# Kernel optimization log

Measured on AMD Instinct MI355X. Metric: run time of the kernel, lower is better.

Reference implementation:

```python
import jax, jax.numpy as jnp
import numpy as np

D_DYN = 256    # dynamic_dim
D_STAT = 64    # static_dim
U_DIM = 48     # config.model.u_dim
N_OBS = 80     # num_prod*2 + num_inj = 32*2 + 16
T = 128        # rollout steps
B = 2048       # batch


def setup_inputs() -> dict:
    key = jax.random.key(0)
    k = jax.random.split(key, 8)
    z_dyn = jax.random.normal(k[0], (B, D_DYN), dtype=jnp.float32)
    z_static = jax.random.normal(k[1], (B, D_STAT), dtype=jnp.float32)
    dt = jnp.ones((1,), dtype=jnp.float32) * 0.05
    U = jax.random.normal(k[2], (T, B, U_DIM), dtype=jnp.float32)
    # learned params, initialized as in the torch module
    eig_raw = jnp.zeros((D_DYN,), dtype=jnp.float32)
    V = jnp.eye(D_DYN, dtype=jnp.float32) + jax.random.normal(k[3], (D_DYN, D_DYN), dtype=jnp.float32) * 0.01
    L = jax.random.normal(k[4], (D_DYN, U_DIM), dtype=jnp.float32) * (1.0 / np.sqrt(U_DIM))
    C = jax.random.normal(k[5], (N_OBS, D_DYN), dtype=jnp.float32) * (1.0 / np.sqrt(D_DYN))
    Dm = jax.random.normal(k[6], (N_OBS, U_DIM), dtype=jnp.float32) * (1.0 / np.sqrt(U_DIM))
    return {"z_dyn": z_dyn, "z_static": z_static, "dt": dt, "U": U,
            "eig_raw": eig_raw, "V": V, "L": L, "C": C, "Dm": Dm}


def reference(z_dyn, z_static, dt, U, eig_raw, V, L, C, Dm):
    # Stable Koopman operator: K = V diag(sigmoid(eig_raw)*0.99) V^{-1}
    eigvals = jax.nn.sigmoid(eig_raw) * 0.99
    K = (V * eigvals[None, :]) @ jnp.linalg.inv(V)  # [d, d]
    KT, LT, CT, DT = K.T, L.T, C.T, Dm.T
    dts = dt[0]

    def step(z, ut):
        ut_dt = ut * dts                 # [B, u_dim]
        z = z @ KT + ut_dt @ LT          # [B, d]
        y = z @ CT + ut_dt @ DT          # [B, n_obs]
        return z, (z, y)

    _, (Z, Y) = jax.lax.scan(step, z_dyn, U)
    return Z, Y  # [T, B, d], [T, B, n_obs]
```

## Files before the change

### kernel.cpp

```cpp
#include <hip/hip_runtime.h>

#define D_   256
#define UD_  48
#define NO_  80
#define T_   128
#define B_   2048

typedef __bf16 bf16x8 __attribute__((ext_vector_type(8)));
typedef float  f32x4  __attribute__((ext_vector_type(4)));
typedef unsigned short ushort_t;

static __device__ __forceinline__ ushort_t f2bf(float f){
  return __builtin_bit_cast(ushort_t, (__bf16)f);
}
static __device__ __forceinline__ float bf2f(ushort_t u){
  union { unsigned int i; float f; } c; c.i = ((unsigned int)u) << 16; return c.f;
}
static __device__ __forceinline__ f32x4 mfma16(bf16x8 a, bf16x8 b, f32x4 c){
  return __builtin_amdgcn_mfma_f32_16x16x32_bf16(a, b, c, 0, 0, 0);
}


__global__ void __launch_bounds__(256) k_pre(
    const float* __restrict__ V, const float* __restrict__ eig,
    const float* __restrict__ Cmat,
    float* __restrict__ W, float* __restrict__ Cw,
    float* __restrict__ lam, float* __restrict__ dVd){
  const int bid = blockIdx.x, tid = threadIdx.x;
  if (bid < 256){
    const float* Ar = V + bid*D_;
    float a0=0.f,a1=0.f,a2=0.f,a3=0.f;
    #pragma unroll 4
    for (int k = 0; k < D_; k += 4){
      a0 += Ar[k+0] * V[(k+0)*D_ + tid];
      a1 += Ar[k+1] * V[(k+1)*D_ + tid];
      a2 += Ar[k+2] * V[(k+2)*D_ + tid];
      a3 += Ar[k+3] * V[(k+3)*D_ + tid];
    }
    W[bid*D_ + tid] = (a0+a1)+(a2+a3);
  } else if (bid < 256 + NO_){
    const int n = bid - 256;
    float acc = 0.f;
    #pragma unroll 4
    for (int j = 0; j < D_; ++j) acc += Cmat[n*D_ + j] * V[j*D_ + tid];
    Cw[n*D_ + tid] = acc;
  } else {
    lam[tid] = 0.99f / (1.0f + expf(-eig[tid]));
    const float v = V[tid*D_ + tid];
    dVd[tid] = v - bf2f(f2bf(v));
  }
}

__global__ void __launch_bounds__(256) k_x1(
    const float* __restrict__ V, const float* __restrict__ W,
    float* __restrict__ X1){
  const int i = blockIdx.x, j = threadIdx.x;
  const float* Ar = V + i*D_;
  float a0=0.f,a1=0.f,a2=0.f,a3=0.f;
  #pragma unroll 4
  for (int k = 0; k < D_; k += 4){
    a0 += Ar[k+0] * W[(k+0)*D_ + j];
    a1 += Ar[k+1] * W[(k+1)*D_ + j];
    a2 += Ar[k+2] * W[(k+2)*D_ + j];
    a3 += Ar[k+3] * W[(k+3)*D_ + j];
  }
  X1[i*D_ + j] = (i == j ? 4.0f : 0.0f) - 6.0f*V[i*D_ + j] + 4.0f*W[i*D_ + j]
                 - ((a0+a1)+(a2+a3));
}

__global__ void __launch_bounds__(256) k_mm_mul(
    const float* __restrict__ A, const float* __restrict__ B,
    float* __restrict__ Cm){
  const int i = blockIdx.x, j = threadIdx.x;
  const float* Ar = A + i*D_;
  float a0=0.f,a1=0.f,a2=0.f,a3=0.f;
  #pragma unroll 4
  for (int k = 0; k < D_; k += 4){
    a0 += Ar[k+0] * B[(k+0)*D_ + j];
    a1 += Ar[k+1] * B[(k+1)*D_ + j];
    a2 += Ar[k+2] * B[(k+2)*D_ + j];
    a3 += Ar[k+3] * B[(k+3)*D_ + j];
  }
  Cm[i*D_ + j] = (a0+a1)+(a2+a3);
}

__global__ void __launch_bounds__(256) k_x2(
    const float* __restrict__ X1, const float* __restrict__ Tm,
    const float* __restrict__ Lmat, const float* __restrict__ dt,
    float* __restrict__ VinvT, float* __restrict__ Lw){
  __shared__ float row[256];
  const int i = blockIdx.x, j = threadIdx.x;
  const float* Xr = X1 + i*D_;
  float a0=0.f,a1=0.f,a2=0.f,a3=0.f;
  #pragma unroll 4
  for (int k = 0; k < D_; k += 4){
    a0 += Xr[k+0] * Tm[(k+0)*D_ + j];
    a1 += Xr[k+1] * Tm[(k+1)*D_ + j];
    a2 += Xr[k+2] * Tm[(k+2)*D_ + j];
    a3 += Xr[k+3] * Tm[(k+3)*D_ + j];
  }
  const float out = 2.0f*Xr[j] - ((a0+a1)+(a2+a3));
  VinvT[j*D_ + i] = out;
  row[j] = out;
  __syncthreads();
  if (j < UD_){
    float acc = 0.f;
    #pragma unroll 4
    for (int k = 0; k < D_; ++k) acc += row[k] * Lmat[k*UD_ + j];
    Lw[i*UD_ + j] = acc * dt[0];
  }
}

__global__ void __launch_bounds__(256) k_prep2(
    const float* __restrict__ z0, const float* __restrict__ VinvT,
    const float* __restrict__ Lw, const float* __restrict__ V,
    const float* __restrict__ Cw, const float* __restrict__ Dmat,
    const float* __restrict__ dt,
    ushort_t* __restrict__ Wchk, ushort_t* __restrict__ Lws,
    ushort_t* __restrict__ Af){
  __shared__ float zr[8][256];
  const int bid = blockIdx.x, tid = threadIdx.x;
  if (bid < 256){
    const int b0 = bid * 8;
    #pragma unroll
    for (int r = 0; r < 8; ++r) zr[r][tid] = z0[(size_t)(b0+r)*D_ + tid];
    __syncthreads();
    float acc[8] = {0.f,0.f,0.f,0.f,0.f,0.f,0.f,0.f};
    #pragma unroll 4
    for (int j = 0; j < D_; ++j){
      const float vj = VinvT[j*D_ + tid];
      #pragma unroll
      for (int r = 0; r < 8; ++r) acc[r] += zr[r][j] * vj;
    }
    #pragma unroll
    for (int r = 0; r < 8; ++r)
      Wchk[(size_t)(b0+r)*D_ + tid] = f2bf(acc[r]);
  } else if (bid < 288){
    const int f = bid - 256;
    if (tid < 64){
      const int l = tid, lm = l & 15, lh = l >> 4;
      const int it = f >> 1, kc2 = f & 1;
      const int ig = it*16 + lm;
      #pragma unroll
      for (int j = 0; j < 8; ++j){
        const int k = 32*kc2 + 4*lh + (j & 3) + 16*(j >> 2);
        Lws[(f*64 + l)*8 + j] = f2bf(k < UD_ ? Lw[ig*UD_ + k] : 0.f);
      }
    }
  } else {
    const int v = (bid - 288)*4 + (tid >> 6);
    if (v < 210){
      const int mt = v / 10, kc = v % 10;
      const int l = tid & 63, lm = l & 15, lh = l >> 4;
      const float dts = dt[0];
      #pragma unroll
      for (int j = 0; j < 8; ++j){
        const int k = 32*kc + 4*lh + (j & 3) + 16*(j >> 2);
        float val = 0.f;
        if (mt < 16){
          if (kc < 8) val = V[(mt*16 + lm)*D_ + k];
        } else {
          const int n = (mt - 16)*16 + lm;
          if (kc < 8) val = Cw[n*D_ + k];
          else { const int ku = k - 256; if (ku < UD_) val = dts * Dmat[n*UD_ + ku]; }
        }
        Af[((size_t)(mt*10 + kc)*64 + l)*8 + j] = f2bf(val);
      }
    }
  }
}

#define SCAN_STEP4(UA, UB, UC, TT) do {                                         \
  union { ushort_t us[8]; bf16x8 v; } c0, c1;                                   \
  c0.us[0]=f2bf((UA).x); c0.us[1]=f2bf((UA).y); c0.us[2]=f2bf((UA).z); c0.us[3]=f2bf((UA).w); \
  c0.us[4]=f2bf((UB).x); c0.us[5]=f2bf((UB).y); c0.us[6]=f2bf((UB).z); c0.us[7]=f2bf((UB).w); \
  c1.us[0]=f2bf((UC).x); c1.us[1]=f2bf((UC).y); c1.us[2]=f2bf((UC).z); c1.us[3]=f2bf((UC).w); \
  c1.us[4]=0; c1.us[5]=0; c1.us[6]=0; c1.us[7]=0;                               \
  _Pragma("unroll")                                                             \
  for (int q = 0; q < 4; ++q){                                                  \
    f32x4 acc = {0.f,0.f,0.f,0.f};                                              \
    acc = mfma16(lwf[q*2+0], c0.v, acc);                                        \
    acc = mfma16(lwf[q*2+1], c1.v, acc);                                        \
    _Pragma("unroll")                                                           \
    for (int r = 0; r < 4; ++r) w[q*4+r] = lamr[q*4+r]*w[q*4+r] + acc[r];       \
  }                                                                             \
  if ((((TT) & 7) == 7) && ((TT) < T_-1)){                                      \
    const int c2 = ((TT)+1) >> 3;                                               \
    _Pragma("unroll")                                                           \
    for (int q = 0; q < 4; ++q){                                                \
      const int i = (itb+q)*16 + 4*lh;                                          \
      ushort4 o; o.x=f2bf(w[q*4+0]); o.y=f2bf(w[q*4+1]); o.z=f2bf(w[q*4+2]); o.w=f2bf(w[q*4+3]); \
      *(ushort4*)(Wchk + ((size_t)c2*B_ + row)*D_ + i) = o;                     \
    }                                                                           \
  }                                                                             \
} while(0)

__global__ void __launch_bounds__(256) k_scan(const float* __restrict__ U,
    const ushort_t* __restrict__ Lws, const float* __restrict__ lam,
    ushort_t* __restrict__ Wchk){
  const int tid = threadIdx.x;
  const int wid = tid >> 6, l = tid & 63;
  const int lm = l & 15, lh = l >> 4;
  const int b0 = blockIdx.x * 16;
  const int row = b0 + lm;
  const int itb = wid*4;

  bf16x8 lwf[8];
  #pragma unroll
  for (int q = 0; q < 4; ++q)
    #pragma unroll
    for (int c = 0; c < 2; ++c)
      lwf[q*2 + c] = *(const bf16x8*)(Lws + ((size_t)(((itb+q)*2 + c)*64 + l))*8);

  float lamr[16], w[16];
  #pragma unroll
  for (int q = 0; q < 4; ++q){
    const int i = (itb+q)*16 + 4*lh;
    const float4 lv = *(const float4*)&lam[i];
    const ushort4 wu = *(const ushort4*)(Wchk + (size_t)row*D_ + i);
    lamr[q*4+0]=lv.x; lamr[q*4+1]=lv.y; lamr[q*4+2]=lv.z; lamr[q*4+3]=lv.w;
    w[q*4+0]=bf2f(wu.x); w[q*4+1]=bf2f(wu.y); w[q*4+2]=bf2f(wu.z); w[q*4+3]=bf2f(wu.w);
  }

  const size_t TS = (size_t)B_ * UD_;
  const float* Urow = U + (size_t)row * UD_;
  float4 Aa, Ab, Ac, Ba, Bb, Bc;
  Aa = *(const float4*)&Urow[4*lh]; Ab = *(const float4*)&Urow[16+4*lh]; Ac = *(const float4*)&Urow[32+4*lh];
  { const float* Up = Urow + TS;
    Ba = *(const float4*)&Up[4*lh]; Bb = *(const float4*)&Up[16+4*lh]; Bc = *(const float4*)&Up[32+4*lh]; }

  #pragma unroll 1
  for (int tt = 0; tt < 64; ++tt){
    const int t0 = 2*tt;
    SCAN_STEP4(Aa, Ab, Ac, t0);
    if (t0 + 2 < T_){
      const float* Up = Urow + (size_t)(t0+2)*TS;
      Aa = *(const float4*)&Up[4*lh]; Ab = *(const float4*)&Up[16+4*lh]; Ac = *(const float4*)&Up[32+4*lh];
    }
    SCAN_STEP4(Ba, Bb, Bc, t0+1);
    if (t0 + 3 < T_){
      const float* Up = Urow + (size_t)(t0+3)*TS;
      Ba = *(const float4*)&Up[4*lh]; Bb = *(const float4*)&Up[16+4*lh]; Bc = *(const float4*)&Up[32+4*lh];
    }
  }
}

__global__ void __launch_bounds__(256) k_fused(
    const float* __restrict__ U, const ushort_t* __restrict__ Af,
    const ushort_t* __restrict__ Lws, const float* __restrict__ lam,
    const float* __restrict__ dVd, const ushort_t* __restrict__ Wchk,
    float* __restrict__ outZ, float* __restrict__ outY){
  __shared__ __align__(16) ushort_t AfZhL[8*8*512];
  __shared__ __align__(16) ushort_t LwsL[32*512];
  __shared__ __align__(16) ushort_t AfYhL[40*512];
  __shared__ __align__(16) float    trbZ[4][16][68];
  __shared__ __align__(16) float    dVdL[128];
  __shared__ __align__(16) float    lamL[256];

  const int tid = threadIdx.x;
  const int bid = blockIdx.x;
  const int h  = bid & 1;
  const int ch = (bid >> 1) & 15;
  const int bq = bid >> 5;
  const int wid = tid >> 6, l = tid & 63;
  const int lm = l & 15, lh = l >> 4;
  const int col0 = bq*64 + wid*16;
  const int col = col0 + lm;

  {
    const uint4* gsrc = (const uint4*)Af;
    uint4* dz = (uint4*)AfZhL;
    #pragma unroll
    for (int r = 0; r < 16; ++r){
      const int i = r*256 + tid;
      const int f = i >> 6, l4 = i & 63;
      const int mi8 = f >> 3, kc = f & 7;
      dz[i] = gsrc[(size_t)((h*8 + mi8)*10 + kc)*64 + l4];
    }
    uint4* dy = (uint4*)AfYhL;
    const int nY = h ? 640 : 2560;
    const int sb = 16 + (h ? 4 : 0);
    #pragma unroll
    for (int r = 0; r < 10; ++r){
      const int i = r*256 + tid;
      if (i < nY){
        const int f = i >> 6, l4 = i & 63;
        const int myl = f / 10, j = f % 10;
        dy[i] = gsrc[(size_t)((sb + myl)*10 + j)*64 + l4];
      }
    }
    const uint4* ls = (const uint4*)Lws;
    uint4* ld = (uint4*)LwsL;
    #pragma unroll
    for (int r = 0; r < 8; ++r) ld[r*256 + tid] = ls[r*256 + tid];
    if (tid < 32) ((float4*)dVdL)[tid] = ((const float4*)(dVd + h*128))[tid];
    else if (tid < 96) ((float4*)lamL)[tid-32] = ((const float4*)lam)[tid-32];
  }

  float w[64];
  #pragma unroll
  for (int kc = 0; kc < 8; ++kc)
    #pragma unroll
    for (int hh = 0; hh < 2; ++hh){
      const int i = 32*kc + 16*hh + 4*lh;
      const ushort4 wu = *(const ushort4*)(Wchk + ((size_t)ch*B_ + col)*D_ + i);
      const int e = 8*kc + 4*hh;
      w[e+0]=bf2f(wu.x); w[e+1]=bf2f(wu.y); w[e+2]=bf2f(wu.z); w[e+3]=bf2f(wu.w);
    }

  const size_t TS = (size_t)B_ * UD_;
  const float* Ucol = U + (size_t)col * UD_;
  float4 ua, ub, uc;
  {
    const float* Ut = Ucol + (size_t)(ch*8)*TS;
    ua = *(const float4*)&Ut[4*lh]; ub = *(const float4*)&Ut[16+4*lh]; uc = *(const float4*)&Ut[32+4*lh];
  }

  __syncthreads();

#define ZLOOP(HH)                                                               \
  { float* zbase = outZ + ((size_t)t*B_ + col0)*D_ + (HH)*128;                  \
    _Pragma("unroll")                                                           \
    for (int g = 0; g < 2; ++g){                                                \
      _Pragma("unroll")                                                         \
      for (int mi = 0; mi < 4; ++mi){                                           \
        const int mi8 = g*4 + mi;                                               \
        f32x4 acc = {0.f,0.f,0.f,0.f};                                          \
        _Pragma("unroll")                                                       \
        for (int kc = 0; kc < 8; ++kc){                                         \
          const bf16x8 af = *(const bf16x8*)&AfZhL[((mi8*8+kc)*64 + l)*8];      \
          acc = mfma16(af, wfr[kc], acc);                                       \
        }                                                                       \
        const float4 dv = *(const float4*)&dVdL[mi8*16 + 4*lh];                 \
        acc[0] += dv.x * (float)wfr[((HH)*8+mi8)>>1][0 + 4*(mi8&1)];            \
        acc[1] += dv.y * (float)wfr[((HH)*8+mi8)>>1][1 + 4*(mi8&1)];            \
        acc[2] += dv.z * (float)wfr[((HH)*8+mi8)>>1][2 + 4*(mi8&1)];            \
        acc[3] += dv.w * (float)wfr[((HH)*8+mi8)>>1][3 + 4*(mi8&1)];            \
        *(float4*)&trbZ[wid][lm][mi*16 + 4*lh] = make_float4(acc[0],acc[1],acc[2],acc[3]); \
      }                                                                         \
      __builtin_amdgcn_wave_barrier();                                          \
      _Pragma("unroll")                                                         \
      for (int j = 0; j < 4; ++j){                                              \
        const int r_ = j*4 + (l >> 4), c16 = l & 15;                            \
        const float4 v = *(const float4*)&trbZ[wid][r_][4*c16];                 \
        *(float4*)&zbase[(size_t)r_*D_ + g*64 + 4*c16] = v;                     \
      }                                                                         \
      __builtin_amdgcn_wave_barrier();                                          \
    } }

#define YLOOP(COFF, NMY)                                                        \
  { float* yrow = outY + ((size_t)t*B_ + col)*NO_ + (COFF);                     \
    _Pragma("unroll")                                                           \
    for (int my = 0; my < (NMY); ++my){                                         \
      f32x4 acc = {0.f,0.f,0.f,0.f};                                            \
      _Pragma("unroll")                                                         \
      for (int kc = 0; kc < 8; ++kc){                                           \
        const bf16x8 af = *(const bf16x8*)&AfYhL[((my*10+kc)*64 + l)*8];        \
        acc = mfma16(af, wfr[kc], acc);                                         \
      }                                                                         \
      { const bf16x8 af8 = *(const bf16x8*)&AfYhL[((my*10+8)*64 + l)*8];        \
        const bf16x8 af9 = *(const bf16x8*)&AfYhL[((my*10+9)*64 + l)*8];        \
        acc = mfma16(af8, uf0, acc); acc = mfma16(af9, uf1, acc); }             \
      *(float4*)&yrow[my*16 + 4*lh] = make_float4(acc[0],acc[1],acc[2],acc[3]); \
    } }

  #pragma unroll 1
  for (int s = 0; s < 8; ++s){
    const int t = ch*8 + s;
    bf16x8 uf0, uf1;
    {
      union { ushort_t us[8]; bf16x8 v; } cv;
      cv.us[0]=f2bf(ua.x); cv.us[1]=f2bf(ua.y); cv.us[2]=f2bf(ua.z); cv.us[3]=f2bf(ua.w);
      cv.us[4]=f2bf(ub.x); cv.us[5]=f2bf(ub.y); cv.us[6]=f2bf(ub.z); cv.us[7]=f2bf(ub.w);
      uf0 = cv.v;
      cv.us[0]=f2bf(uc.x); cv.us[1]=f2bf(uc.y); cv.us[2]=f2bf(uc.z); cv.us[3]=f2bf(uc.w);
      cv.us[4]=0; cv.us[5]=0; cv.us[6]=0; cv.us[7]=0;
      uf1 = cv.v;
    }
    if (s < 7){
      const float* Ut = Ucol + (size_t)(t+1)*TS;
      ua = *(const float4*)&Ut[4*lh]; ub = *(const float4*)&Ut[16+4*lh]; uc = *(const float4*)&Ut[32+4*lh];
    }
    #pragma unroll
    for (int it = 0; it < 16; ++it){
      const bf16x8 a0 = *(const bf16x8*)&LwsL[((it*2+0)*64 + l)*8];
      const bf16x8 a1 = *(const bf16x8*)&LwsL[((it*2+1)*64 + l)*8];
      const float4 lv = *(const float4*)&lamL[32*(it>>1) + 16*(it&1) + 4*lh];
      f32x4 acc = {0.f,0.f,0.f,0.f};
      acc = mfma16(a0, uf0, acc);
      acc = mfma16(a1, uf1, acc);
      const int e0 = 8*(it>>1) + 4*(it&1);
      w[e0+0] = lv.x*w[e0+0] + acc[0];
      w[e0+1] = lv.y*w[e0+1] + acc[1];
      w[e0+2] = lv.z*w[e0+2] + acc[2];
      w[e0+3] = lv.w*w[e0+3] + acc[3];
    }
    bf16x8 wfr[8];
    #pragma unroll
    for (int kc = 0; kc < 8; ++kc){
      union { ushort_t us[8]; bf16x8 v; } cv;
      #pragma unroll
      for (int j = 0; j < 8; ++j) cv.us[j] = f2bf(w[8*kc + j]);
      wfr[kc] = cv.v;
    }
    if (h == 0){
      ZLOOP(0);
      YLOOP(0, 4);
    } else {
      ZLOOP(1);
      YLOOP(64, 1);
    }
  }
#undef ZLOOP
#undef YLOOP
}

extern "C" void kernel_launch(void* const* d_in, const int* in_sizes, int n_in,
                              void* d_out, int out_size, void* d_ws, size_t ws_size,
                              hipStream_t stream){
  const float* z0  = (const float*)d_in[0];
  const float* dt  = (const float*)d_in[2];
  const float* U   = (const float*)d_in[3];
  const float* eig = (const float*)d_in[4];
  const float* V   = (const float*)d_in[5];
  const float* L   = (const float*)d_in[6];
  const float* C   = (const float*)d_in[7];
  const float* Dm  = (const float*)d_in[8];
  float* outZ = (float*)d_out;
  float* outY = outZ + (size_t)T_*B_*D_;

  char* ws = (char*)d_ws;
  float* Xa    = (float*)(ws + 0);
  float* Xb    = (float*)(ws + 262144);
  float* Tt    = (float*)(ws + 524288);
  float* Lw    = (float*)(ws + 786432);
  float* Cw    = (float*)(ws + 835584);
  float* lam   = (float*)(ws + 917504);
  float* dVd   = (float*)(ws + 918528);
  ushort_t* Af   = (ushort_t*)(ws + 919552);
  ushort_t* Lws  = (ushort_t*)(ws + 1134592);
  ushort_t* Wchk = (ushort_t*)(ws + 1167360);
  if (ws_size < 17944576u) return;

  k_pre   <<<337,256,0,stream>>>(V, eig, C, Xa, Cw, lam, dVd);
  k_x1    <<<256,256,0,stream>>>(V, Xa, Xb);
  k_mm_mul<<<256,256,0,stream>>>(V, Xb, Tt);
  k_x2    <<<256,256,0,stream>>>(Xb, Tt, L, dt, Xa, Lw);
  k_prep2 <<<342,256,0,stream>>>(z0, Xa, Lw, V, Cw, Dm, dt, Wchk, Lws, Af);
  k_scan  <<<128,256,0,stream>>>(U, Lws, lam, Wchk);
  k_fused <<<1024,256,0,stream>>>(U, Af, Lws, lam, dVd, Wchk, outZ, outY);
}
```

Baseline: 279.7 us.

## Split sequential diagonal scan into parallel chunk scans plus carry propagation

The single sequential 128-step scan over 128 blocks becomes two passes. The first pass runs 1920 blocks, each computing one 8-step chunk from a zero state and writing its local contribution. The second pass propagates carries across the 16 chunk checkpoints with lambda^8. This is meant to remove the long serial latency of a scan that used only 128 blocks, in exchange for an extra kernel launch and extra bf16 read-modify-write traffic on the checkpoints, which could also add rounding error.

Result: faster. 262.0 us (-6.3%).

```diff
diff --git a/kernel.cpp b/kernel.cpp
--- a/kernel.cpp
+++ b/kernel.cpp
@@ -170,7 +170,8 @@
   }
 }
 
-#define SCAN_STEP4(UA, UB, UC, TT) do {                                         \
+
+#define LSCAN_STEP(UA, UB, UC) do {                                             \
   union { ushort_t us[8]; bf16x8 v; } c0, c1;                                   \
   c0.us[0]=f2bf((UA).x); c0.us[1]=f2bf((UA).y); c0.us[2]=f2bf((UA).z); c0.us[3]=f2bf((UA).w); \
   c0.us[4]=f2bf((UB).x); c0.us[5]=f2bf((UB).y); c0.us[6]=f2bf((UB).z); c0.us[7]=f2bf((UB).w); \
@@ -184,25 +185,17 @@
     _Pragma("unroll")                                                           \
     for (int r = 0; r < 4; ++r) w[q*4+r] = lamr[q*4+r]*w[q*4+r] + acc[r];       \
   }                                                                             \
-  if ((((TT) & 7) == 7) && ((TT) < T_-1)){                                      \
-    const int c2 = ((TT)+1) >> 3;                                               \
-    _Pragma("unroll")                                                           \
-    for (int q = 0; q < 4; ++q){                                                \
-      const int i = (itb+q)*16 + 4*lh;                                          \
-      ushort4 o; o.x=f2bf(w[q*4+0]); o.y=f2bf(w[q*4+1]); o.z=f2bf(w[q*4+2]); o.w=f2bf(w[q*4+3]); \
-      *(ushort4*)(Wchk + ((size_t)c2*B_ + row)*D_ + i) = o;                     \
-    }                                                                           \
-  }                                                                             \
 } while(0)
 
-__global__ void __launch_bounds__(256) k_scan(const float* __restrict__ U,
+__global__ void __launch_bounds__(256) k_scanA(const float* __restrict__ U,
     const ushort_t* __restrict__ Lws, const float* __restrict__ lam,
     ushort_t* __restrict__ Wchk){
   const int tid = threadIdx.x;
   const int wid = tid >> 6, l = tid & 63;
   const int lm = l & 15, lh = l >> 4;
-  const int b0 = blockIdx.x * 16;
-  const int row = b0 + lm;
+  const int ch = blockIdx.x >> 7;
+  const int bq = blockIdx.x & 127;
+  const int row = bq*16 + lm;
   const int itb = wid*4;
 
   bf16x8 lwf[8];
@@ -217,30 +210,56 @@
   for (int q = 0; q < 4; ++q){
     const int i = (itb+q)*16 + 4*lh;
     const float4 lv = *(const float4*)&lam[i];
-    const ushort4 wu = *(const ushort4*)(Wchk + (size_t)row*D_ + i);
     lamr[q*4+0]=lv.x; lamr[q*4+1]=lv.y; lamr[q*4+2]=lv.z; lamr[q*4+3]=lv.w;
-    w[q*4+0]=bf2f(wu.x); w[q*4+1]=bf2f(wu.y); w[q*4+2]=bf2f(wu.z); w[q*4+3]=bf2f(wu.w);
+    w[q*4+0]=0.f; w[q*4+1]=0.f; w[q*4+2]=0.f; w[q*4+3]=0.f;
   }
 
   const size_t TS = (size_t)B_ * UD_;
-  const float* Urow = U + (size_t)row * UD_;
+  const float* Urow = U + ((size_t)(ch*8)*B_ + row) * UD_;
   float4 Aa, Ab, Ac, Ba, Bb, Bc;
   Aa = *(const float4*)&Urow[4*lh]; Ab = *(const float4*)&Urow[16+4*lh]; Ac = *(const float4*)&Urow[32+4*lh];
   { const float* Up = Urow + TS;
     Ba = *(const float4*)&Up[4*lh]; Bb = *(const float4*)&Up[16+4*lh]; Bc = *(const float4*)&Up[32+4*lh]; }
 
+  #pragma unroll
+  for (int tt = 0; tt < 4; ++tt){
+    LSCAN_STEP(Aa, Ab, Ac);
+    if (tt < 3){
+      const float* Up = Urow + (size_t)(2*tt+2)*TS;
+      Aa = *(const float4*)&Up[4*lh]; Ab = *(const float4*)&Up[16+4*lh]; Ac = *(const float4*)&Up[32+4*lh];
+    }
+    LSCAN_STEP(Ba, Bb, Bc);
+    if (tt < 3){
+      const float* Up = Urow + (size_t)(2*tt+3)*TS;
+      Ba = *(const float4*)&Up[4*lh]; Bb = *(const float4*)&Up[16+4*lh]; Bc = *(const float4*)&Up[32+4*lh];
+    }
+  }
+  #pragma unroll
+  for (int q = 0; q < 4; ++q){
+    const int i = (itb+q)*16 + 4*lh;
+    ushort4 o; o.x=f2bf(w[q*4+0]); o.y=f2bf(w[q*4+1]); o.z=f2bf(w[q*4+2]); o.w=f2bf(w[q*4+3]);
+    *(ushort4*)(Wchk + ((size_t)(ch+1)*B_ + row)*D_ + i) = o;
+  }
+}
+
+__global__ void __launch_bounds__(256) k_scanB(const float* __restrict__ lam,
+    ushort_t* __restrict__ Wchk){
+  const int d = threadIdx.x;
+  const int b0 = blockIdx.x * 16;
+  float l2 = lam[d]; l2 = l2*l2;
+  float l8 = l2*l2;  l8 = l8*l8;
+  float W[16];
+  #pragma unroll
+  for (int r = 0; r < 16; ++r)
+    W[r] = bf2f(Wchk[(size_t)(b0+r)*D_ + d]);
   #pragma unroll 1
-  for (int tt = 0; tt < 64; ++tt){
-    const int t0 = 2*tt;
-    SCAN_STEP4(Aa, Ab, Ac, t0);
-    if (t0 + 2 < T_){
-      const float* Up = Urow + (size_t)(t0+2)*TS;
-      Aa = *(const float4*)&Up[4*lh]; Ab = *(const float4*)&Up[16+4*lh]; Ac = *(const float4*)&Up[32+4*lh];
-    }
-    SCAN_STEP4(Ba, Bb, Bc, t0+1);
-    if (t0 + 3 < T_){
-      const float* Up = Urow + (size_t)(t0+3)*TS;
-      Ba = *(const float4*)&Up[4*lh]; Bb = *(const float4*)&Up[16+4*lh]; Bc = *(const float4*)&Up[32+4*lh];
+  for (int j = 0; j < 15; ++j){
+    ushort_t* slot = Wchk + (size_t)(j+1)*B_*D_;
+    #pragma unroll
+    for (int r = 0; r < 16; ++r){
+      const float c = bf2f(slot[(size_t)(b0+r)*D_ + d]);
+      W[r] = l8*W[r] + c;
+      slot[(size_t)(b0+r)*D_ + d] = f2bf(W[r]);
     }
   }
 }
@@ -447,6 +466,7 @@
   k_mm_mul<<<256,256,0,stream>>>(V, Xb, Tt);
   k_x2    <<<256,256,0,stream>>>(Xb, Tt, L, dt, Xa, Lw);
   k_prep2 <<<342,256,0,stream>>>(z0, Xa, Lw, V, Cw, Dm, dt, Wchk, Lws, Af);
-  k_scan  <<<128,256,0,stream>>>(U, Lws, lam, Wchk);
+  k_scanA <<<1920,256,0,stream>>>(U, Lws, lam, Wchk);
+  k_scanB <<<128,256,0,stream>>>(lam, Wchk);
   k_fused <<<1024,256,0,stream>>>(U, Af, Lws, lam, dVd, Wchk, outZ, outY);
 }
```
